# Kernel optimization log

Hardware: AMD Instinct MI355X
Metric: run time of the kernel (lower is better)

## Reference

```python
import jax, jax.numpy as jnp
import numpy as np
from jax import lax

VOCAB = 32000
N_E = 1024
N_D = 1024
DEPTH = 4
L = 512
B = 8
HIGHWAY_BIAS = -3.0  # args.bias, folded into forget-gate bias


def setup_inputs() -> dict:
    key = jax.random.key(0)
    ks = jax.random.split(key, 8)
    x = jax.random.randint(ks[0], (L, B), 0, VOCAB)
    hidden = jnp.zeros((DEPTH, B, N_D), dtype=jnp.float32)
    emb = jax.random.normal(ks[1], (VOCAB, N_E), dtype=jnp.float32) * (3.0 / VOCAB) ** 0.5
    W0 = jax.random.normal(ks[2], (N_E, 4 * N_D), dtype=jnp.float32) * N_E ** -0.5
    Wl = jax.random.normal(ks[3], (DEPTH - 1, N_D, 3 * N_D), dtype=jnp.float32) * N_D ** -0.5
    vc = jax.random.normal(ks[4], (DEPTH, 2 * N_D), dtype=jnp.float32) * 0.1
    out_W = jax.random.normal(ks[5], (N_D, VOCAB), dtype=jnp.float32) * (3.0 / VOCAB) ** 0.5
    out_b = jnp.zeros((VOCAB,), dtype=jnp.float32)
    return {"x": x, "hidden": hidden, "emb": emb, "W0": W0, "Wl": Wl,
            "vc": vc, "out_W": out_W, "out_b": out_b}


def _sru_layer(u0, u1, u2, resid, vf, vr, c0):
    # u*: (L, B, d) precomputed GEMM outputs; scan only does elementwise recurrence.
    def step(c, inp):
        u0t, u1t, u2t, rt = inp
        f = jax.nn.sigmoid(u1t + vf * c + HIGHWAY_BIAS)
        r = jax.nn.sigmoid(u2t + vr * c)
        c_new = f * c + (1.0 - f) * u0t
        h = r * c_new + (1.0 - r) * rt
        return c_new, h
    c_last, hs = lax.scan(step, c0, (u0, u1, u2, resid))
    return hs, c_last


def reference(x, hidden, emb, W0, Wl, vc, out_W, out_b):
    h = emb[x]  # (L, B, n_e); dropout disabled (p=0)
    c_finals = []
    for layer in range(DEPTH):
        if layer == 0:
            U = jnp.einsum('lbe,ek->lbk', h, W0).reshape(L, B, 4, N_D)
            resid = U[:, :, 3]  # k=4: transformed input as highway residual
        else:
            U = jnp.einsum('lbd,dk->lbk', h, Wl[layer - 1]).reshape(L, B, 3, N_D)
            resid = h           # k=3: highway residual is the layer input
        vf = vc[layer, :N_D]
        vr = vc[layer, N_D:]
        h, c_last = _sru_layer(U[:, :, 0], U[:, :, 1], U[:, :, 2], resid, vf, vr, hidden[layer])
        c_finals.append(c_last)
    out = h.reshape(L * B, N_D) @ out_W + out_b  # (L*B, vocab)
    return out, jnp.stack(c_finals)
```

## Files before the change

### kernel.cpp

```cpp
#include <hip/hip_runtime.h>
#include <hip/hip_bf16.h>

#define L_SEQ 512
#define BATCH 8
#define ND 1024
#define VOCAB_N 32000
#define MROWS 4096
#define KDIM 1024
#define BK 64
#define NKT (KDIM / BK)
#define NKS 32
#define NSCAN 128

typedef unsigned short u16;
typedef unsigned int u32;
using bf16x8 = __attribute__((ext_vector_type(8))) __bf16;
using f32x4  = __attribute__((ext_vector_type(4))) float;
using u16x8  = __attribute__((ext_vector_type(8))) unsigned short;
using u16x4  = __attribute__((ext_vector_type(4))) unsigned short;

#define BAR() asm volatile("s_barrier" ::: "memory")
#define VMW(n) asm volatile("s_waitcnt vmcnt(" #n ")" ::: "memory")
#define SCHED() __builtin_amdgcn_sched_barrier(0)

static __device__ __forceinline__ u16 f2bf(float f) {
  u32 u = __builtin_bit_cast(u32, f);
  u32 r = u + 0x7FFF + ((u >> 16) & 1);
  return (u16)(r >> 16);
}
static __device__ __forceinline__ float bf2f(u16 b) {
  u32 u = ((u32)b) << 16;
  return __builtin_bit_cast(float, u);
}
static __device__ __forceinline__ void gload16(const void* g, void* l) {
  __builtin_amdgcn_global_load_lds(
      (const __attribute__((address_space(1))) void*)g,
      (__attribute__((address_space(3))) void*)l, 16, 0, 0);
}

static __device__ __forceinline__ void transpose_body(int tb, const float* __restrict__ W,
                                                      u16* __restrict__ Wt, int Ndim) {
  __shared__ float s[32][33];
  int nx = Ndim >> 5;
  int n0 = (tb % nx) * 32, k0 = (tb / nx) * 32;
  int tid = threadIdx.x;
  int tx = tid & 31, ty = tid >> 5;
#pragma unroll
  for (int i = 0; i < 4; i++)
    s[ty * 4 + i][tx] = __builtin_nontemporal_load(
        &W[(size_t)(k0 + ty * 4 + i) * Ndim + n0 + tx]);
  __syncthreads();
  int n = tid >> 3, kg = tid & 7;
  u16x4 o;
#pragma unroll
  for (int j = 0; j < 4; j++) o[j] = f2bf(s[kg * 4 + j][n]);
  *(u16x4*)(Wt + (size_t)(n0 + n) * KDIM + k0 + kg * 4) = o;
}

__global__ __launch_bounds__(256) void k_embed_t(const int* __restrict__ x,
                                                 const float* __restrict__ emb,
                                                 u16* __restrict__ h,
                                                 const float* __restrict__ Wsrc,
                                                 u16* __restrict__ WtOut, int NdimT) {
  if (blockIdx.x >= 2048) {
    transpose_body(blockIdx.x - 2048, Wsrc, WtOut, NdimT);
    return;
  }
  int t = blockIdx.x * 256 + threadIdx.x;
  int fidx = t * 8;
  int row = fidx >> 10;
  int col = fidx & 1023;
  int tok = x[row];
  const float4* src = (const float4*)(emb + (size_t)tok * ND + col);
  float4 a = src[0], b = src[1];
  u16x8 o;
  o[0]=f2bf(a.x); o[1]=f2bf(a.y); o[2]=f2bf(a.z); o[3]=f2bf(a.w);
  o[4]=f2bf(b.x); o[5]=f2bf(b.y); o[6]=f2bf(b.z); o[7]=f2bf(b.w);
  *(u16x8*)(h + fidx) = o;
}

__global__ __launch_bounds__(256) void k_transpose_cast(const float* __restrict__ W,
                                                        u16* __restrict__ Wt, int Ndim) {
  transpose_body(blockIdx.x, W, Wt, Ndim);
}

static __device__ __forceinline__ void stage8k(const u16* __restrict__ gbase,
                                               char* sm, int qdst, int tid) {
#pragma unroll
  for (int j = 0; j < 2; ++j) {
    int d = (j * 256 + tid) * 16;
    int o = d ^ (((d >> 7) & 7) << 4);
    gload16(gbase + (size_t)(o >> 7) * KDIM + ((o & 127) >> 1), sm + qdst + d);
  }
}

static __device__ __forceinline__ bf16x8 frag_ld(const char* sm, int base, int r, int cb) {
  int p = (r * 128 + cb) ^ ((r & 7) << 4);
  return *(const bf16x8*)(sm + base + p);
}

static __device__ __forceinline__ bf16x8 frag32(const char* smbase, int r, int cb) {
  int p = r * 64 + cb;
  p ^= ((p >> 7) & 3) << 4;
  return *(const bf16x8*)(smbase + p);
}

__global__ __launch_bounds__(256, 2) void k_gemm_out(const u16* __restrict__ A,
                                                     const u16* __restrict__ Bt,
                                                     float* __restrict__ CoutF, int Ndim,
                                                     const float* __restrict__ bias) {
  extern __shared__ __align__(16) char sm[];

  int cpx = gridDim.x >> 3;
  int bid = blockIdx.x;
  int wg = (bid & 7) * cpx + (bid >> 3);
  int bm = wg & 31;
  int bn = wg >> 5;
  int m0 = bm * 128, n0 = bn * 256;

  int tid = threadIdx.x;
  int lane = tid & 63, w = tid >> 6;
  int l15 = lane & 15, hi16 = lane >> 4;

  f32x4 acc[8][4] = {};
  bf16x8 aA[8], bB[4];

  const u16* Ab = A + (size_t)m0 * KDIM;
  const u16* Bb = Bt + (size_t)n0 * KDIM;

  auto stage = [&](int t, int base) {
#pragma unroll
    for (int j = 0; j < 2; ++j) {
      int d = (j * 256 + tid) * 16;
      int o = d ^ (((d >> 7) & 3) << 4);
      gload16(Ab + (size_t)(o >> 6) * KDIM + t * 32 + ((o & 63) >> 1),
              sm + base + d);
    }
#pragma unroll
    for (int j = 0; j < 4; ++j) {
      int d = (j * 256 + tid) * 16;
      int o = d ^ (((d >> 7) & 3) << 4);
      gload16(Bb + (size_t)(o >> 6) * KDIM + t * 32 + ((o & 63) >> 1),
              sm + base + 8192 + d);
    }
  };

  stage(0, 0);
  stage(1, 24576);
  VMW(6);
  BAR();

  const int cb = hi16 * 16;

  int rb = 0, sb = 2;
#pragma unroll 1
  for (int t = 0; t < NKS; ++t) {
    if (t + 2 < NKS) stage(t + 2, sb * 24576);
    const char* cur = sm + rb * 24576;
#pragma unroll
    for (int mi = 0; mi < 8; ++mi) aA[mi] = frag32(cur, mi * 16 + l15, cb);
#pragma unroll
    for (int ni = 0; ni < 4; ++ni) bB[ni] = frag32(cur + 8192, w * 64 + ni * 16 + l15, cb);
    __builtin_amdgcn_s_setprio(1);
#pragma unroll
    for (int mi = 0; mi < 8; ++mi)
#pragma unroll
      for (int ni = 0; ni < 4; ++ni)
        acc[mi][ni] = __builtin_amdgcn_mfma_f32_16x16x32_bf16(aA[mi], bB[ni], acc[mi][ni], 0, 0, 0);
    __builtin_amdgcn_s_setprio(0);
    SCHED();
    if (t + 2 < NKS) { VMW(6); } else { VMW(0); }
    BAR();
    rb = (rb == 2) ? 0 : rb + 1;
    sb = (sb == 2) ? 0 : sb + 1;
  }

  float* epi = (float*)sm;
  for (int p = 0; p < 4; ++p) {
    if (p) __syncthreads();
    if (w == p) {
#pragma unroll
      for (int mi = 0; mi < 8; ++mi)
#pragma unroll
        for (int ni = 0; ni < 4; ++ni)
#pragma unroll
          for (int r = 0; r < 4; ++r)
            epi[(mi * 16 + hi16 * 4 + r) * 68 + ni * 16 + l15] = acc[mi][ni][r];
    }
    __syncthreads();
    int gcolbase = n0 + p * 64;
#pragma unroll
    for (int i = 0; i < 8; ++i) {
      int fidx = i * 1024 + tid * 4;
      int row = fidx >> 6, col = fidx & 63;
      f32x4 v = *(const f32x4*)(epi + row * 68 + col);
      int gcol = gcolbase + col;
      const float4 bb = *(const float4*)(bias + gcol);
      v[0] += bb.x; v[1] += bb.y; v[2] += bb.z; v[3] += bb.w;
      __builtin_nontemporal_store(v, (f32x4*)(CoutF + (size_t)(m0 + row) * Ndim + gcol));
    }
  }
}

template <int EPI>
__global__ __launch_bounds__(256, 2) void k_gemm128(const u16* __restrict__ A,
                                                    const u16* __restrict__ Bt,
                                                    u16* __restrict__ Cout, int Ndim) {
  extern __shared__ __align__(16) char sm[];

  int cpx = gridDim.x >> 3;
  int bid = blockIdx.x;
  int wg = (bid & 7) * cpx + (bid >> 3);
  int bm = wg & 31;
  int bn = wg >> 5;
  int m0 = bm * 128, n0 = bn * 128;

  int tid = threadIdx.x;
  int lane = tid & 63, w = tid >> 6;
  int wm = w >> 1, wn = w & 1;
  int l15 = lane & 15, hi16 = lane >> 4;
  const int rA = wm * 64 + l15, rB = wn * 64 + l15;

  f32x4 acc[4][4] = {};
  bf16x8 aA[4][2], bB[4][2];

  const u16* Ab = A + (size_t)m0 * KDIM;
  const u16* Bb = Bt + (size_t)n0 * KDIM;

  auto stage_tile = [&](int t, int buf) {
    int base = buf * 32768;
    stage8k(Ab + t * 64,                     sm, base,         tid);
    stage8k(Ab + (size_t)64 * KDIM + t * 64, sm, base + 8192,  tid);
    stage8k(Bb + t * 64,                     sm, base + 16384, tid);
    stage8k(Bb + (size_t)64 * KDIM + t * 64, sm, base + 24576, tid);
  };

  stage_tile(0, 0);
  VMW(0);
  BAR();

#pragma unroll 1
  for (int t = 0; t < NKT; ++t) {
    int cur = (t & 1) * 32768;
    if (t + 1 < NKT) stage_tile(t + 1, (t & 1) ^ 1);
#pragma unroll
    for (int kk = 0; kk < 2; ++kk) {
      int cb = kk * 64 + hi16 * 16;
#pragma unroll
      for (int mi = 0; mi < 4; ++mi) aA[mi][kk] = frag_ld(sm, cur, rA + mi * 16, cb);
#pragma unroll
      for (int ni = 0; ni < 4; ++ni) bB[ni][kk] = frag_ld(sm, cur + 16384, rB + ni * 16, cb);
    }
    __builtin_amdgcn_s_setprio(1);
#pragma unroll
    for (int kk = 0; kk < 2; ++kk)
#pragma unroll
      for (int mi = 0; mi < 4; ++mi)
#pragma unroll
        for (int ni = 0; ni < 4; ++ni)
          acc[mi][ni] = __builtin_amdgcn_mfma_f32_16x16x32_bf16(aA[mi][kk], bB[ni][kk], acc[mi][ni], 0, 0, 0);
    __builtin_amdgcn_s_setprio(0);
    SCHED();
    VMW(0);
    BAR();
  }

  float* epi = (float*)sm;
  for (int p = 0; p < 2; ++p) {
    if (p) __syncthreads();
    if (wn == p) {
#pragma unroll
      for (int mi = 0; mi < 4; ++mi)
#pragma unroll
        for (int ni = 0; ni < 4; ++ni)
#pragma unroll
          for (int r = 0; r < 4; ++r)
            epi[(wm * 64 + mi * 16 + hi16 * 4 + r) * 68 + ni * 16 + l15] = acc[mi][ni][r];
    }
    __syncthreads();
    int gcolbase = n0 + p * 64;
    int plane = gcolbase >> 10;
#pragma unroll
    for (int i = 0; i < 8; ++i) {
      int fidx = i * 1024 + tid * 4;
      int row = fidx >> 6, col = fidx & 63;
      f32x4 v = *(const f32x4*)(epi + row * 68 + col);
      int gcol = gcolbase + col;
      if (plane == 1) {
#pragma unroll
        for (int j = 0; j < 4; j++) v[j] = -1.44269504f * (v[j] - 3.0f);
      } else if (plane == 2) {
#pragma unroll
        for (int j = 0; j < 4; j++) v[j] = -1.44269504f * v[j];
      }
      u16x4 o;
#pragma unroll
      for (int j = 0; j < 4; j++) o[j] = f2bf(v[j]);
      *(u16x4*)(Cout + (size_t)(m0 + row) * Ndim + gcol) = o;
    }
  }
}

__global__ __launch_bounds__(256) void k_scan(const u16* __restrict__ U, int P,
                                              const u16* __restrict__ resid, int rstride,
                                              u16* __restrict__ hout,
                                              const float* __restrict__ vc,
                                              const float* __restrict__ hidden,
                                              float* __restrict__ cfin, int layer,
                                              const float* __restrict__ Wsrc,
                                              u16* __restrict__ WtOut, int NdimT) {
  if (blockIdx.x >= NSCAN) {
    transpose_body(blockIdx.x - NSCAN, Wsrc, WtOut, NdimT);
    return;
  }
  if (threadIdx.x >= 64) return;
  int cid = blockIdx.x * 64 + threadIdx.x;
  int b = cid >> 10, d = cid & 1023;
  float vfp = -1.44269504f * vc[layer * 2048 + d];
  float vrp = -1.44269504f * vc[layer * 2048 + 1024 + d];
  float c = hidden[layer * 8192 + cid];
  const u16* pu = U + (size_t)b * P * 1024 + d;
  const u16* pr = resid + (size_t)b * rstride + d;
  u16* ph = hout + (size_t)b * 1024 + d;
  const int ustep = P * 1024;
  const int rstep = rstride;

  u16 su0[16], sa1[16], sa2[16], srs[16];
#pragma unroll
  for (int j = 0; j < 16; j++) {
    su0[j] = pu[(size_t)(8 * j) * ustep];
    sa1[j] = pu[(size_t)(8 * j) * ustep + 1024];
    sa2[j] = pu[(size_t)(8 * j) * ustep + 2048];
    srs[j] = pr[(size_t)(8 * j) * rstep];
  }
  for (int tb = 0; tb < L_SEQ; tb += 16) {
#pragma unroll
    for (int j = 0; j < 16; j++) {
      int t = tb + j;
      float u0f = bf2f(su0[j]), a1f = bf2f(sa1[j]);
      float a2f = bf2f(sa2[j]), rf = bf2f(srs[j]);
      int tp = (t + 16) & 511;
      su0[j] = pu[(size_t)(8 * tp) * ustep];
      sa1[j] = pu[(size_t)(8 * tp) * ustep + 1024];
      sa2[j] = pu[(size_t)(8 * tp) * ustep + 2048];
      srs[j] = pr[(size_t)(8 * tp) * rstep];
      float e1 = __builtin_amdgcn_exp2f(fmaf(vfp, c, a1f));
      float e2 = __builtin_amdgcn_exp2f(fmaf(vrp, c, a2f));
      float fv = __builtin_amdgcn_rcpf(1.0f + e1);
      float rv = __builtin_amdgcn_rcpf(1.0f + e2);
      float cn = fmaf(fv, c - u0f, u0f);
      float hv = fmaf(rv, cn - rf, rf);
      ph[(size_t)t * (BATCH * ND)] = f2bf(hv);
      c = cn;
    }
  }
  cfin[layer * 8192 + cid] = c;
}

extern "C" void kernel_launch(void* const* d_in, const int* in_sizes, int n_in,
                              void* d_out, int out_size, void* d_ws, size_t ws_size,
                              hipStream_t stream) {
  const int*   x      = (const int*)d_in[0];
  const float* hidden = (const float*)d_in[1];
  const float* emb    = (const float*)d_in[2];
  const float* W0     = (const float*)d_in[3];
  const float* Wl     = (const float*)d_in[4];
  const float* vc     = (const float*)d_in[5];
  const float* outW   = (const float*)d_in[6];
  const float* outb   = (const float*)d_in[7];
  float* out = (float*)d_out;

  char* ws = (char*)d_ws;
  u16* hA    = (u16*)ws;
  u16* hB    = (u16*)(ws + 8388608);
  u16* U     = (u16*)(ws + 16777216);
  u16* Wt    = (u16*)(ws + 50331648);
  float* cfin = out + (size_t)MROWS * VOCAB_N;

  const size_t wtbig_off_big = 58720256;
  bool bigws = ws_size >= (size_t)(wtbig_off_big + (size_t)VOCAB_N * KDIM * 2);
  u16* WtBig = (u16*)(ws + (bigws ? wtbig_off_big : 16777216));

  k_embed_t<<<2048 + 4096, 256, 0, stream>>>(x, emb, hA, W0, Wt, 4096);

  k_gemm128<0><<<32 * 32, 256, 65536, stream>>>(hA, Wt, U, 4096);
  k_scan<<<NSCAN + 3072, 256, 0, stream>>>(U, 4, U + 3 * 1024, 4 * 1024, hB, vc, hidden,
                                           cfin, 0, Wl, Wt, 3072);

  const u16* hin[3]  = {hB, hA, hB};
  u16*       hout[3] = {hA, hB, hA};
  for (int l = 1; l <= 3; l++) {
    k_gemm128<1><<<32 * 24, 256, 65536, stream>>>(hin[l - 1], Wt, U, 3072);
    if (l < 3) {
      k_scan<<<NSCAN + 3072, 256, 0, stream>>>(U, 3, hin[l - 1], 1024, hout[l - 1], vc,
                                               hidden, cfin, l,
                                               Wl + (size_t)l * KDIM * 3072, Wt, 3072);
    } else if (bigws) {
      k_scan<<<NSCAN + 32000, 256, 0, stream>>>(U, 3, hin[l - 1], 1024, hout[l - 1], vc,
                                                hidden, cfin, l, outW, WtBig, VOCAB_N);
    } else {
      k_scan<<<NSCAN, 256, 0, stream>>>(U, 3, hin[l - 1], 1024, hout[l - 1], vc,
                                        hidden, cfin, l, nullptr, nullptr, 32);
      k_transpose_cast<<<32000, 256, 0, stream>>>(outW, WtBig, VOCAB_N);
    }
  }

  k_gemm_out<<<32 * 125, 256, 73728, stream>>>(hA, WtBig, out, VOCAB_N, outb);
}
```

Measured before the change: 686.4 us.

## Interleave LDS fragment loads, global prefetch and MFMA in four phases

Splits each K-step of the output GEMM main loop into four phases. Each phase loads part of the A/B fragments from LDS, issues a slice of the next-next tile's global-to-LDS copies, and runs a quarter of the MFMAs, with barriers between phases. The aim is to spread memory traffic across the MFMA work so LDS reads and global loads overlap with matrix compute, in the style of a ping-pong schedule. It adds many extra barriers and lgkmcnt waits per iteration, which could serialize the waves more than before.

```diff
diff --git a/kernel.cpp b/kernel.cpp
--- a/kernel.cpp
+++ b/kernel.cpp
@@ -21,6 +21,7 @@
 
 #define BAR() asm volatile("s_barrier" ::: "memory")
 #define VMW(n) asm volatile("s_waitcnt vmcnt(" #n ")" ::: "memory")
+#define LGKM0() asm volatile("s_waitcnt lgkmcnt(0)" ::: "memory")
 #define SCHED() __builtin_amdgcn_sched_barrier(0)
 
 static __device__ __forceinline__ u16 f2bf(float f) {
@@ -128,16 +129,17 @@
   const u16* Ab = A + (size_t)m0 * KDIM;
   const u16* Bb = Bt + (size_t)n0 * KDIM;
 
-  auto stage = [&](int t, int base) {
+  auto stageA = [&](int t, int base) {
 #pragma unroll
     for (int j = 0; j < 2; ++j) {
       int d = (j * 256 + tid) * 16;
       int o = d ^ (((d >> 7) & 3) << 4);
-      gload16(Ab + (size_t)(o >> 6) * KDIM + t * 32 + ((o & 63) >> 1),
-              sm + base + d);
-    }
-#pragma unroll
-    for (int j = 0; j < 4; ++j) {
+      gload16(Ab + (size_t)(o >> 6) * KDIM + t * 32 + ((o & 63) >> 1), sm + base + d);
+    }
+  };
+  auto stageB = [&](int t, int base, int h) {
+#pragma unroll
+    for (int j = 2 * h; j < 2 * h + 2; ++j) {
       int d = (j * 256 + tid) * 16;
       int o = d ^ (((d >> 7) & 3) << 4);
       gload16(Bb + (size_t)(o >> 6) * KDIM + t * 32 + ((o & 63) >> 1),
@@ -145,35 +147,63 @@
     }
   };
 
-  stage(0, 0);
-  stage(1, 24576);
+  stageA(0, 0); stageB(0, 0, 0); stageB(0, 0, 1);
+  stageA(1, 24576); stageB(1, 24576, 0); stageB(1, 24576, 1);
   VMW(6);
   BAR();
 
   const int cb = hi16 * 16;
+
+#define MFMA_C(M0, N0)                                                         \
+  __builtin_amdgcn_s_setprio(1);                                               \
+  _Pragma("unroll") for (int mi = (M0); mi < (M0) + 4; ++mi)                   \
+  _Pragma("unroll") for (int ni = (N0); ni < (N0) + 2; ++ni)                   \
+      acc[mi][ni] = __builtin_amdgcn_mfma_f32_16x16x32_bf16(                   \
+          aA[mi], bB[ni], acc[mi][ni], 0, 0, 0);                               \
+  __builtin_amdgcn_s_setprio(0);                                               \
+  SCHED();
 
   int rb = 0, sb = 2;
 #pragma unroll 1
   for (int t = 0; t < NKS; ++t) {
-    if (t + 2 < NKS) stage(t + 2, sb * 24576);
     const char* cur = sm + rb * 24576;
-#pragma unroll
-    for (int mi = 0; mi < 8; ++mi) aA[mi] = frag32(cur, mi * 16 + l15, cb);
-#pragma unroll
-    for (int ni = 0; ni < 4; ++ni) bB[ni] = frag32(cur + 8192, w * 64 + ni * 16 + l15, cb);
-    __builtin_amdgcn_s_setprio(1);
-#pragma unroll
-    for (int mi = 0; mi < 8; ++mi)
-#pragma unroll
-      for (int ni = 0; ni < 4; ++ni)
-        acc[mi][ni] = __builtin_amdgcn_mfma_f32_16x16x32_bf16(aA[mi], bB[ni], acc[mi][ni], 0, 0, 0);
-    __builtin_amdgcn_s_setprio(0);
-    SCHED();
-    if (t + 2 < NKS) { VMW(6); } else { VMW(0); }
-    BAR();
+    const bool st = (t + 2 < NKS);
+    const int sbase = sb * 24576;
+
+#pragma unroll
+    for (int mi = 0; mi < 4; ++mi) aA[mi] = frag32(cur, mi * 16 + l15, cb);
+#pragma unroll
+    for (int ni = 0; ni < 2; ++ni) bB[ni] = frag32(cur + 8192, w * 64 + ni * 16 + l15, cb);
+    if (st) stageA(t + 2, sbase);
+    BAR();
+    LGKM0(); SCHED();
+    MFMA_C(0, 0);
+    BAR();
+
+#pragma unroll
+    for (int ni = 2; ni < 4; ++ni) bB[ni] = frag32(cur + 8192, w * 64 + ni * 16 + l15, cb);
+    if (st) stageB(t + 2, sbase, 0);
+    BAR();
+    LGKM0(); SCHED();
+    MFMA_C(0, 2);
+    BAR();
+
+#pragma unroll
+    for (int mi = 4; mi < 8; ++mi) aA[mi] = frag32(cur, mi * 16 + l15, cb);
+    if (st) stageB(t + 2, sbase, 1);
+    BAR();
+    LGKM0(); SCHED();
+    MFMA_C(4, 0);
+    BAR();
+
+    MFMA_C(4, 2);
+    if (st) { VMW(6); } else { VMW(0); }
+    BAR();
+
     rb = (rb == 2) ? 0 : rb + 1;
     sb = (sb == 2) ? 0 : sb + 1;
   }
+#undef MFMA_C
 
   float* epi = (float*)sm;
   for (int p = 0; p < 4; ++p) {
```

Result: no change. 694.0 us (+1.1%).
